# Optimization experiments

Hardware: AMD Instinct MI355X
Metric: run time of the kernel (lower is better)

Reference implementation:

```python
import jax, jax.numpy as jnp
import numpy as np

N = 100000
F_IN = 128
E = 1_600_000
NEG_SLOPE = 0.2  # PyG GATConv default negative_slope


def _seg_sum(v, idx, n):
    return jax.ops.segment_sum(v, idx, num_segments=n)


def gcn_conv(x, W, b, src, dst, n):
    # PyG GCNConv: D^{-1/2} (A + I) D^{-1/2} X W + b (self loops already in src/dst)
    h = x @ W
    deg = _seg_sum(jnp.ones(src.shape, h.dtype), dst, n)
    dinv = jnp.where(deg > 0, jax.lax.rsqrt(deg), 0.0)
    norm = dinv[src] * dinv[dst]  # [E]
    return _seg_sum(h[src] * norm[:, None], dst, n) + b


def gat_conv(x, W, a_src, a_dst, b, src, dst, n, heads, out_ch):
    # PyG GATConv (concat=True), eval mode (dropout inactive)
    h = (x @ W).reshape(n, heads, out_ch)          # [n,H,C]
    s = jnp.einsum('nhc,hc->nh', h, a_src)          # per-node src score
    t = jnp.einsum('nhc,hc->nh', h, a_dst)          # per-node dst score
    e = jax.nn.leaky_relu(s[src] + t[dst], NEG_SLOPE)  # [E,H]
    m = jax.ops.segment_max(e, dst, num_segments=n)    # stable segment softmax
    m = jnp.where(jnp.isfinite(m), m, 0.0)
    p = jnp.exp(e - m[dst])
    denom = _seg_sum(p, dst, n)
    alpha = p / (denom[dst] + 1e-16)                 # [E,H]
    out = _seg_sum(h[src] * alpha[:, :, None], dst, n)  # [n,H,C]
    return out.reshape(n, heads * out_ch) + b


def setup_inputs():
    key = jax.random.key(0)
    ks = jax.random.split(key, 24)
    x = jax.random.normal(ks[0], (N, F_IN), jnp.float32) * 0.1
    half = N // 2
    # one-hot user/item type flags read by forward (x[:,0]==1 / x[:,1]==1)
    x = x.at[:, 0].set(0.0).at[:, 1].set(0.0)
    x = x.at[:half, 0].set(1.0).at[half:, 1].set(1.0)
    src = jax.random.randint(ks[1], (E,), 0, N, dtype=jnp.int32)
    dst = jax.random.randint(ks[2], (E,), 0, N, dtype=jnp.int32)
    edge_index = jnp.stack([src, dst])

    def p(k, shape):
        return jax.random.normal(k, shape, jnp.float32) * 0.1

    inp = {"x": x, "edge_index": edge_index,
           "gcn_w": p(ks[3], (F_IN, 16)), "gcn_b": jnp.zeros((16,), jnp.float32)}
    dims = [(16, 16, 8), (128, 16, 8), (128, 16, 8), (128, 2, 1)]
    for i, (fi, fo, h) in enumerate(dims, start=1):
        inp[f"g{i}_w"] = p(ks[3 + 4 * i], (fi, h * fo))
        inp[f"g{i}_as"] = p(ks[4 + 4 * i], (h, fo))
        inp[f"g{i}_ad"] = p(ks[5 + 4 * i], (h, fo))
        inp[f"g{i}_b"] = jnp.zeros((h * fo,), jnp.float32)
    return inp


def reference(x, edge_index, gcn_w, gcn_b,
              g1_w, g1_as, g1_ad, g1_b,
              g2_w, g2_as, g2_ad, g2_b,
              g3_w, g3_as, g3_ad, g3_b,
              g4_w, g4_as, g4_ad, g4_b):
    n = x.shape[0]
    loops = jnp.arange(n, dtype=edge_index.dtype)  # self loops (added by GCN/GAT layers)
    src = jnp.concatenate([edge_index[0], loops])
    dst = jnp.concatenate([edge_index[1], loops])
    h = jax.nn.elu(gcn_conv(x, gcn_w, gcn_b, src, dst, n))
    h = jax.nn.elu(gat_conv(h, g1_w, g1_as, g1_ad, g1_b, src, dst, n, 8, 16))
    h = jax.nn.elu(gat_conv(h, g2_w, g2_as, g2_ad, g2_b, src, dst, n, 8, 16))
    h = jax.nn.elu(gat_conv(h, g3_w, g3_as, g3_ad, g3_b, src, dst, n, 8, 16))
    h = jax.nn.elu(gat_conv(h, g4_w, g4_as, g4_ad, g4_b, src, dst, n, 1, 2))  # [n,2]
    half = n // 2  # users are rows [:half], items rows [half:]
    out = jnp.concatenate([h[:half], h[half:]], axis=1)  # [half,4]
    return jax.nn.log_softmax(out, axis=1)
```

## Files before the change

kernel.cpp:

```cpp
#include <hip/hip_runtime.h>
#include <cstddef>
#include <cstdint>

#define NN 100000
#define NPAD 100032
#define NE 1600000
#define ET (NE + NN)
#define ETP_MAX (ET + 8 * NN)
#define HALFN (NN / 2)
#define NEG_SLOPE 0.2f
#define SCB 1024
#define RP 8
#define RNODES (NN / RP)
#define CHUNK 8192

typedef __attribute__((ext_vector_type(8))) short short8v;
typedef __attribute__((ext_vector_type(4))) float float4v;
typedef __attribute__((ext_vector_type(2))) float float2v;

__device__ __forceinline__ float lrelu(float x) { return x > 0.f ? x : NEG_SLOPE * x; }

__device__ __forceinline__ uint16_t f2bf(float f) {
  uint32_t u = __float_as_uint(f);
  uint32_t r = u + 0x7fffu + ((u >> 16) & 1u);
  return (uint16_t)(r >> 16);
}
__device__ __forceinline__ float bflo(uint32_t u) { return __uint_as_float(u << 16); }
__device__ __forceinline__ float bfhi(uint32_t u) { return __uint_as_float(u & 0xffff0000u); }

template<int K, int M>
__launch_bounds__(256)
__global__ void gemm4_kernel(const float* __restrict__ X, const float* __restrict__ W,
                             float* __restrict__ Y, int n) {
  constexpr int CG = M / 4;
  constexpr int RG = 256 / CG;
  constexpr int RPT = 2;
  constexpr int RT = RG * RPT;
  constexpr int KP = K + 1;
  __shared__ __align__(16) float sW[K * M];
  __shared__ float sX[RT * KP];
  for (int i = threadIdx.x; i < K * M; i += 256) sW[i] = W[i];
  const int jg = threadIdx.x % CG;
  const int rg = threadIdx.x / CG;
  const int r0 = rg * RPT;
  for (int base = blockIdx.x * RT; base < n; base += gridDim.x * RT) {
    __syncthreads();
    const int nrows = (n - base) < RT ? (n - base) : RT;
    for (int i = threadIdx.x; i < nrows * K; i += 256) {
      int r = i / K, c = i - r * K;
      sX[r * KP + c] = X[(size_t)base * K + i];
    }
    __syncthreads();
    float acc[RPT][4];
    #pragma unroll
    for (int rr = 0; rr < RPT; ++rr) acc[rr][0] = acc[rr][1] = acc[rr][2] = acc[rr][3] = 0.f;
    #pragma unroll 4
    for (int k = 0; k < K; ++k) {
      const float4 w = *(const float4*)&sW[k * M + jg * 4];
      #pragma unroll
      for (int rr = 0; rr < RPT; ++rr) {
        const float xv = sX[(r0 + rr) * KP + k];
        acc[rr][0] = fmaf(xv, w.x, acc[rr][0]);
        acc[rr][1] = fmaf(xv, w.y, acc[rr][1]);
        acc[rr][2] = fmaf(xv, w.z, acc[rr][2]);
        acc[rr][3] = fmaf(xv, w.w, acc[rr][3]);
      }
    }
    #pragma unroll
    for (int rr = 0; rr < RPT; ++rr) {
      if (r0 + rr < nrows) {
        float4 o = make_float4(acc[rr][0], acc[rr][1], acc[rr][2], acc[rr][3]);
        *(float4*)&Y[(size_t)(base + r0 + rr) * M + jg * 4] = o;
      }
    }
  }
}

template<int KB>
__launch_bounds__(256)
__global__ void wpack_kernel(const float* __restrict__ W, uint16_t* __restrict__ wp,
                             int Kreal) {
  int tid = blockIdx.x * 256 + threadIdx.x;
  if (tid >= KB * 8 * 64) return;
  int lane = tid & 63;
  int ctkb = tid >> 6;
  int kb = ctkb % KB, ct = ctkb / KB;
  int nc = ct * 16 + (lane & 15);
  int k0 = kb * 32 + (lane >> 4) * 8;
  ushort4 o0, o1;
  uint16_t v[8];
  #pragma unroll
  for (int j = 0; j < 8; ++j) {
    int k = k0 + j;
    v[j] = (k < Kreal) ? f2bf(W[(size_t)k * 128 + nc]) : (uint16_t)0;
  }
  o0.x = v[0]; o0.y = v[1]; o0.z = v[2]; o0.w = v[3];
  o1.x = v[4]; o1.y = v[5]; o1.z = v[6]; o1.w = v[7];
  *(ushort4*)&wp[(size_t)tid * 8] = o0;
  *(ushort4*)&wp[(size_t)tid * 8 + 4] = o1;
}

template<int KB, int XS>
__launch_bounds__(256)
__global__ void gemm_mfma_kernel(const uint16_t* __restrict__ X,
                                 const uint16_t* __restrict__ wp,
                                 const float* __restrict__ aS, const float* __restrict__ aD,
                                 uint16_t* __restrict__ Y,
                                 float* __restrict__ S, float* __restrict__ T, int n) {
  __shared__ float sC[4][16 * 136];
  const int wv = threadIdx.x >> 6;
  const int lane = threadIdx.x & 63;
  const int rowbase = blockIdx.x * 64 + wv * 16;
  int arow = rowbase + (lane & 15);
  if (arow >= n) arow = n - 1;
  const uint16_t* xp = X + (size_t)arow * XS + ((lane >> 4) * 8);
  short8v a[KB];
  #pragma unroll
  for (int kb = 0; kb < KB; ++kb) a[kb] = *(const short8v*)(xp + kb * 32);
  #pragma unroll
  for (int ct = 0; ct < 8; ++ct) {
    float4v acc = {0.f, 0.f, 0.f, 0.f};
    #pragma unroll
    for (int kb = 0; kb < KB; ++kb) {
      short8v b = *(const short8v*)&wp[(size_t)((ct * KB + kb) * 64 + lane) * 8];
      acc = __builtin_amdgcn_mfma_f32_16x16x32_bf16(a[kb], b, acc, 0, 0, 0);
    }
    #pragma unroll
    for (int r = 0; r < 4; ++r)
      sC[wv][((lane >> 4) * 4 + r) * 136 + ct * 16 + (lane & 15)] = acc[r];
  }
  #pragma unroll
  for (int t = 0; t < 4; ++t) {
    int idx = t * 64 + lane;
    int row = idx >> 4;
    int c8 = idx & 15;
    const float* pr = &sC[wv][row * 136 + c8 * 8];
    float4 lo = *(const float4*)pr;
    float4 hi = *(const float4*)(pr + 4);
    uint4 o;
    o.x = (uint32_t)f2bf(lo.x) | ((uint32_t)f2bf(lo.y) << 16);
    o.y = (uint32_t)f2bf(lo.z) | ((uint32_t)f2bf(lo.w) << 16);
    o.z = (uint32_t)f2bf(hi.x) | ((uint32_t)f2bf(hi.y) << 16);
    o.w = (uint32_t)f2bf(hi.z) | ((uint32_t)f2bf(hi.w) << 16);
    *(uint4*)&Y[(size_t)(rowbase + row) * 128 + c8 * 8] = o;
  }
  {
    int r = lane & 15;
    int hg = lane >> 4;
    int node = rowbase + r;
    if (node < n) {
      #pragma unroll
      for (int hh = 0; hh < 2; ++hh) {
        int h = hg * 2 + hh;
        float sv = 0.f, tv = 0.f;
        #pragma unroll
        for (int c = 0; c < 16; ++c) {
          float v = sC[wv][r * 136 + h * 16 + c];
          sv = fmaf(v, aS[h * 16 + c], sv);
          tv = fmaf(v, aD[h * 16 + c], tv);
        }
        S[(size_t)node * 8 + h] = sv;
        T[(size_t)node * 8 + h] = tv;
      }
    }
  }
}

template<int K, int ROWS>
__launch_bounds__(256)
__global__ void gemm_s2_kernel(const uint16_t* __restrict__ Xb, const float* __restrict__ W,
                               const float* __restrict__ aS, const float* __restrict__ aD,
                               float* __restrict__ Y, float* __restrict__ S,
                               float* __restrict__ T, int n) {
  constexpr int KP = K + 1;
  __shared__ float sW[K * 2];
  __shared__ float sX[ROWS * KP];
  if (blockIdx.x == 0 && threadIdx.x == 0) {
    S[NN] = -1e30f; T[NN] = 0.f;
    Y[(size_t)NN * 2] = 0.f; Y[(size_t)NN * 2 + 1] = 0.f;
  }
  for (int i = threadIdx.x; i < K * 2; i += 256) sW[i] = W[i];
  const float as0 = aS[0], as1 = aS[1], ad0 = aD[0], ad1 = aD[1];
  for (int base = blockIdx.x * ROWS; base < n; base += gridDim.x * ROWS) {
    __syncthreads();
    const int nrows = (n - base) < ROWS ? (n - base) : ROWS;
    for (int i = threadIdx.x; i < nrows * (K / 4); i += 256) {
      int r = i / (K / 4), c = i - r * (K / 4);
      uint2 u = *(const uint2*)&Xb[(size_t)(base + r) * K + c * 4];
      sX[r * KP + c * 4 + 0] = bflo(u.x);
      sX[r * KP + c * 4 + 1] = bfhi(u.x);
      sX[r * KP + c * 4 + 2] = bflo(u.y);
      sX[r * KP + c * 4 + 3] = bfhi(u.y);
    }
    __syncthreads();
    for (int r = threadIdx.x; r < nrows; r += 256) {
      float a0 = 0.f, a1 = 0.f;
      #pragma unroll 4
      for (int k = 0; k < K; ++k) {
        float xv = sX[r * KP + k];
        a0 = fmaf(xv, sW[k * 2], a0);
        a1 = fmaf(xv, sW[k * 2 + 1], a1);
      }
      int node = base + r;
      float2 o; o.x = a0; o.y = a1;
      *(float2*)&Y[(size_t)node * 2] = o;
      S[node] = a0 * as0 + a1 * as1;
      T[node] = a0 * ad0 + a1 * ad1;
    }
  }
}

__launch_bounds__(256)
__global__ void rank_kernel(const int* __restrict__ edst, int* __restrict__ cursor,
                            int* __restrict__ rank) {
  int e = blockIdx.x * 256 + threadIdx.x;
  if (e >= ET) return;
  int dn = e < NE ? edst[e] : e - NE;
  rank[e] = atomicAdd(&cursor[dn], 1);
}

__device__ __forceinline__ int pad8(int d) { return (d + 7) & ~7; }

__launch_bounds__(256)
__global__ void scan1_kernel(const int* __restrict__ degi, int* __restrict__ rowptr,
                             int* __restrict__ bsums) {
  __shared__ int sd[256];
  int t = threadIdx.x;
  int base = blockIdx.x * SCB + t * 4;
  int v0 = base + 0 < NN ? pad8(degi[base + 0]) : 0;
  int v1 = base + 1 < NN ? pad8(degi[base + 1]) : 0;
  int v2 = base + 2 < NN ? pad8(degi[base + 2]) : 0;
  int v3 = base + 3 < NN ? pad8(degi[base + 3]) : 0;
  int s = v0 + v1 + v2 + v3;
  sd[t] = s;
  __syncthreads();
  for (int off = 1; off < 256; off <<= 1) {
    int x = (t >= off) ? sd[t - off] : 0;
    __syncthreads();
    sd[t] += x;
    __syncthreads();
  }
  int excl = sd[t] - s;
  if (t == 255) bsums[blockIdx.x] = sd[255];
  if (base + 0 < NN) rowptr[base + 0] = excl;
  excl += v0;
  if (base + 1 < NN) rowptr[base + 1] = excl;
  excl += v1;
  if (base + 2 < NN) rowptr[base + 2] = excl;
  excl += v2;
  if (base + 3 < NN) rowptr[base + 3] = excl;
}

__launch_bounds__(256)
__global__ void scan2_kernel(int* __restrict__ bsums, int nb) {
  __shared__ int sd[256];
  int t = threadIdx.x;
  int v = t < nb ? bsums[t] : 0;
  sd[t] = v;
  __syncthreads();
  for (int off = 1; off < 256; off <<= 1) {
    int x = (t >= off) ? sd[t - off] : 0;
    __syncthreads();
    sd[t] += x;
    __syncthreads();
  }
  if (t < nb) bsums[t] = sd[t] - v;
  if (t == nb - 1) bsums[nb] = sd[t];
}

__launch_bounds__(256)
__global__ void scan3_kernel(int* __restrict__ rowptr, const int* __restrict__ bsums, int nb) {
  int i = blockIdx.x * 256 + threadIdx.x;
  if (i < NN) rowptr[i] += bsums[i / SCB];
  if (i == 0) rowptr[NN] = bsums[nb];
}

__launch_bounds__(256)
__global__ void dinv_kernel(const int* __restrict__ deg, float* __restrict__ dinv,
                            float* __restrict__ S8, float* __restrict__ T8) {
  int i = blockIdx.x * 256 + threadIdx.x;
  if (i > NN) return;
  if (i == NN) {
    dinv[i] = 0.f;
    #pragma unroll
    for (int h = 0; h < 8; ++h) {
      S8[(size_t)NN * 8 + h] = -1e30f;
      T8[(size_t)NN * 8 + h] = 0.f;
    }
    return;
  }
  int d = deg[i];
  dinv[i] = d > 0 ? rsqrtf((float)d) : 0.f;
}

__launch_bounds__(256)
__global__ void padfill_kernel(const int* __restrict__ rowptr, const int* __restrict__ deg,
                               int* __restrict__ csr) {
  int i = blockIdx.x * 256 + threadIdx.x;
  if (i >= NN) return;
  int e = rowptr[i] + deg[i], e1 = rowptr[i + 1];
  for (; e < e1; ++e) csr[e] = NN;
}

__launch_bounds__(256)
__global__ void scatter_part_kernel(const int* __restrict__ esrc, const int* __restrict__ edst,
                                    const int* __restrict__ rowptr, const int* __restrict__ rank,
                                    int* __restrict__ csr_src) {
  int p = blockIdx.x & (RP - 1);
  int c = blockIdx.x >> 3;
  int lo = p * RNODES, hi = lo + RNODES;
  int e0 = c * CHUNK;
  int e1 = e0 + CHUNK < ET ? e0 + CHUNK : ET;
  for (int e = e0 + threadIdx.x; e < e1; e += 256) {
    int dn = e < NE ? edst[e] : e - NE;
    if (dn >= lo && dn < hi) {
      int sn = e < NE ? esrc[e] : e - NE;
      csr_src[rowptr[dn] + rank[e]] = sn;
    }
  }
}

__launch_bounds__(256)
__global__ void fused_gat_kernel(const int* __restrict__ rowptr, const int* __restrict__ csr,
                                 const float* __restrict__ S, const float* __restrict__ T,
                                 const uint16_t* __restrict__ Hm, const float* __restrict__ bias,
                                 uint16_t* __restrict__ Outb) {
  const int lane = threadIdx.x & 63;
  const int d = (blockIdx.x * 256 + threadIdx.x) >> 6;
  if (d >= NN) return;
  const int rs = rowptr[d];
  const int deg = rowptr[d + 1] - rs;
  const int eg = lane >> 4;
  const int cl = lane & 15;
  const int hp = cl >> 1;
  const float Th = T[(size_t)d * 8 + hp];
  const char* sb = (const char*)S;
  const char* hb = (const char*)Hm;
  float m = -1e38f;
  float s = 0.f;
  float2v A0 = {0.f, 0.f}, A1 = {0.f, 0.f}, A2 = {0.f, 0.f}, A3 = {0.f, 0.f};
  const uint32_t clo = (uint32_t)(cl << 4);
  const uint32_t hpo = (uint32_t)(hp << 2);
  int iA = rs + eg;
  int snA = csr[iA];
  int snB = csr[iA + 4];
  for (int l0 = 0; l0 < deg; l0 += 8) {
    int snA2 = csr[iA + 8];
    int snB2 = csr[iA + 12];
    uint4 uA = *(const uint4*)(hb + (((uint32_t)snA << 8) + clo));
    uint4 uB = *(const uint4*)(hb + (((uint32_t)snB << 8) + clo));
    float svA = *(const float*)(sb + (((uint32_t)snA << 5) + hpo));
    float svB = *(const float*)(sb + (((uint32_t)snB << 5) + hpo));
    iA += 8;
    float eA = lrelu(svA + Th);
    float eB = lrelu(svB + Th);
    float nm = fmaxf(m, fmaxf(eA, eB));
    if (nm > m) {
      float sc = __expf(m - nm);
      float2v scv = {sc, sc};
      s *= sc;
      A0 *= scv; A1 *= scv; A2 *= scv; A3 *= scv;
      m = nm;
    }
    float pA = __expf(eA - m);
    float pB = __expf(eB - m);
    s += pA + pB;
    float2v ppA = {pA, pA}, ppB = {pB, pB};
    A0 = ppA * (float2v){bflo(uA.x), bfhi(uA.x)} + A0;
    A1 = ppA * (float2v){bflo(uA.y), bfhi(uA.y)} + A1;
    A2 = ppA * (float2v){bflo(uA.z), bfhi(uA.z)} + A2;
    A3 = ppA * (float2v){bflo(uA.w), bfhi(uA.w)} + A3;
    A0 = ppB * (float2v){bflo(uB.x), bfhi(uB.x)} + A0;
    A1 = ppB * (float2v){bflo(uB.y), bfhi(uB.y)} + A1;
    A2 = ppB * (float2v){bflo(uB.z), bfhi(uB.z)} + A2;
    A3 = ppB * (float2v){bflo(uB.w), bfhi(uB.w)} + A3;
    snA = snA2; snB = snB2;
  }
  #pragma unroll
  for (int mask = 16; mask <= 32; mask <<= 1) {
    float om = __shfl_xor(m, mask);
    float os = __shfl_xor(s, mask);
    float o0x = __shfl_xor(A0.x, mask), o0y = __shfl_xor(A0.y, mask);
    float o1x = __shfl_xor(A1.x, mask), o1y = __shfl_xor(A1.y, mask);
    float o2x = __shfl_xor(A2.x, mask), o2y = __shfl_xor(A2.y, mask);
    float o3x = __shfl_xor(A3.x, mask), o3y = __shfl_xor(A3.y, mask);
    float nm = fmaxf(m, om);
    float s1 = __expf(m - nm), s2 = __expf(om - nm);
    s = s * s1 + os * s2;
    A0.x = A0.x * s1 + o0x * s2; A0.y = A0.y * s1 + o0y * s2;
    A1.x = A1.x * s1 + o1x * s2; A1.y = A1.y * s1 + o1y * s2;
    A2.x = A2.x * s1 + o2x * s2; A2.y = A2.y * s1 + o2y * s2;
    A3.x = A3.x * s1 + o3x * s2; A3.y = A3.y * s1 + o3y * s2;
    m = nm;
  }
  {
    float2v Blo = (eg & 1) ? A1 : A0;
    float2v Bhi = (eg & 1) ? A3 : A2;
    float2v B = (eg & 2) ? Bhi : Blo;
    const float inv = 1.f / (s + 1e-16f);
    float2 b = *(const float2*)&bias[cl * 8 + eg * 2];
    float v0 = fmaf(B.x, inv, b.x);
    float v1 = fmaf(B.y, inv, b.y);
    v0 = v0 > 0.f ? v0 : expm1f(v0);
    v1 = v1 > 0.f ? v1 : expm1f(v1);
    uint32_t o = (uint32_t)f2bf(v0) | ((uint32_t)f2bf(v1) << 16);
    *(uint32_t*)&Outb[(size_t)d * 128 + cl * 8 + eg * 2] = o;
  }
}

__launch_bounds__(256)
__global__ void fused_gat1_kernel(const int* __restrict__ rowptr, const int* __restrict__ csr,
                                  const float* __restrict__ S, const float* __restrict__ T,
                                  const float* __restrict__ Hm2, const float* __restrict__ bias,
                                  float* __restrict__ Out) {
  int lane = threadIdx.x & 63;
  int sub = lane >> 4, l16 = lane & 15;
  int d = ((blockIdx.x * 256 + threadIdx.x) >> 6) * 4 + sub;
  if (d >= NN) return;
  int rs = rowptr[d], deg = rowptr[d + 1] - rs;
  float Td = T[d];
  float m = -1e38f, sAcc = 0.f, a0 = 0.f, a1 = 0.f;
  for (int l = l16; l < deg; l += 16) {
    int sn = csr[rs + l];
    float2 hv = *(const float2*)&Hm2[(size_t)sn * 2];
    float sv = S[sn];
    float e = lrelu(sv + Td);
    float nm = fmaxf(m, e);
    if (e > m) {
      float sc = __expf(m - nm);
      sAcc *= sc; a0 *= sc; a1 *= sc; m = nm;
    }
    float p = __expf(e - m);
    sAcc += p;
    a0 = fmaf(p, hv.x, a0);
    a1 = fmaf(p, hv.y, a1);
  }
  #pragma unroll
  for (int mask = 1; mask <= 8; mask <<= 1) {
    float om = __shfl_xor(m, mask);
    float os = __shfl_xor(sAcc, mask);
    float oa0 = __shfl_xor(a0, mask);
    float oa1 = __shfl_xor(a1, mask);
    float nm = fmaxf(m, om);
    float s1 = __expf(m - nm), s2 = __expf(om - nm);
    sAcc = sAcc * s1 + os * s2;
    a0 = a0 * s1 + oa0 * s2;
    a1 = a1 * s1 + oa1 * s2;
    m = nm;
  }
  if (l16 == 0) {
    float inv = 1.f / (sAcc + 1e-16f);
    float v0 = fmaf(a0, inv, bias[0]);
    float v1 = fmaf(a1, inv, bias[1]);
    v0 = v0 > 0.f ? v0 : expm1f(v0);
    v1 = v1 > 0.f ? v1 : expm1f(v1);
    float2 o; o.x = v0; o.y = v1;
    *(float2*)&Out[(size_t)d * 2] = o;
  }
}

__launch_bounds__(256)
__global__ void gcn_pull_kernel(const int* __restrict__ rowptr, const int* __restrict__ csr_src,
                                const float* __restrict__ dinv, const float* __restrict__ Hm,
                                const float* __restrict__ bias, uint16_t* __restrict__ Outb) {
  int d = blockIdx.x * 16 + threadIdx.x / 16;
  if (d >= NN) return;
  int f = threadIdx.x & 15;
  int rs = rowptr[d], re = rowptr[d + 1];
  float acc = 0.f;
  int j = rs;
  for (; j + 4 <= re; j += 4) {
    int s0 = csr_src[j], s1 = csr_src[j + 1], s2 = csr_src[j + 2], s3 = csr_src[j + 3];
    float d0 = dinv[s0], d1 = dinv[s1], d2 = dinv[s2], d3 = dinv[s3];
    float h0 = Hm[(size_t)s0 * 16 + f], h1 = Hm[(size_t)s1 * 16 + f];
    float h2 = Hm[(size_t)s2 * 16 + f], h3 = Hm[(size_t)s3 * 16 + f];
    acc = fmaf(d0, h0, acc); acc = fmaf(d1, h1, acc);
    acc = fmaf(d2, h2, acc); acc = fmaf(d3, h3, acc);
  }
  for (; j < re; ++j) {
    int sn = csr_src[j];
    acc = fmaf(dinv[sn], Hm[(size_t)sn * 16 + f], acc);
  }
  float v = acc * dinv[d] + bias[f];
  v = v > 0.f ? v : expm1f(v);
  Outb[(size_t)d * 32 + f] = f2bf(v);
  Outb[(size_t)d * 32 + 16 + f] = 0;
}

__launch_bounds__(256)
__global__ void final_kernel(const float* __restrict__ A, float* __restrict__ Out) {
  int i = blockIdx.x * 256 + threadIdx.x;
  if (i >= HALFN) return;
  float v0 = A[(size_t)i * 2 + 0];
  float v1 = A[(size_t)i * 2 + 1];
  float v2 = A[(size_t)(i + HALFN) * 2 + 0];
  float v3 = A[(size_t)(i + HALFN) * 2 + 1];
  float m = fmaxf(fmaxf(v0, v1), fmaxf(v2, v3));
  float e0 = __expf(v0 - m), e1 = __expf(v1 - m), e2 = __expf(v2 - m), e3 = __expf(v3 - m);
  float l = logf(e0 + e1 + e2 + e3) + m;
  Out[(size_t)i * 4 + 0] = v0 - l;
  Out[(size_t)i * 4 + 1] = v1 - l;
  Out[(size_t)i * 4 + 2] = v2 - l;
  Out[(size_t)i * 4 + 3] = v3 - l;
}

extern "C" void kernel_launch(void* const* d_in, const int* in_sizes, int n_in,
                              void* d_out, int out_size, void* d_ws, size_t ws_size,
                              hipStream_t stream) {
  const float* x     = (const float*)d_in[0];
  const int*   eidx  = (const int*)d_in[1];
  const int*   esrc  = eidx;
  const int*   edst  = eidx + NE;
  const float* gcn_w = (const float*)d_in[2];
  const float* gcn_b = (const float*)d_in[3];

  char* ws = (char*)d_ws;
  uint16_t* hbf    = (uint16_t*)(ws + 0);
  uint16_t* bufAb  = (uint16_t*)(ws + 25700000);
  uint16_t* gcnHbf = (uint16_t*)(ws + 51400000);
  float*    bufB   = (float*)   (ws + 57900000);
  float*    bufC   = (float*)   (ws + 64400000);
  float*    Sb     = (float*)   (ws + 65300000);
  float*    Tb     = (float*)   (ws + 68600000);
  int*      rowptr = (int*)     (ws + 151900000);
  int*      cursor = (int*)     (ws + 152300008);
  int*      csr    = (int*)     (ws + 152700008);
  float*    dinv   = (float*)   (ws + 162700008);
  int*      bsums  = (int*)     (ws + 163100016);
  int*      rank   = (int*)     (ws + 163100528);
  uint16_t* wpck   = (uint16_t*)(ws + 169900528);

  constexpr int NB_SCAN = (NN + SCB - 1) / SCB;

  hipMemsetAsync(cursor, 0, (size_t)NN * 4, stream);
  rank_kernel<<<(ET + 255) / 256, 256, 0, stream>>>(edst, cursor, rank);
  scan1_kernel<<<NB_SCAN, 256, 0, stream>>>(cursor, rowptr, bsums);
  scan2_kernel<<<1, 256, 0, stream>>>(bsums, NB_SCAN);
  scan3_kernel<<<(NN + 256) / 256, 256, 0, stream>>>(rowptr, bsums, NB_SCAN);
  dinv_kernel<<<(NN + 256) / 256, 256, 0, stream>>>(cursor, dinv, Sb, Tb);
  padfill_kernel<<<(NN + 255) / 256, 256, 0, stream>>>(rowptr, cursor, csr);
  {
    int nch = (ET + CHUNK - 1) / CHUNK;
    scatter_part_kernel<<<nch * RP, 256, 0, stream>>>(esrc, edst, rowptr, rank, csr);
  }

  {
    int tiles = (NN + 127) / 128;
    if (tiles > 4096) tiles = 4096;
    gemm4_kernel<128, 16><<<tiles, 256, 0, stream>>>(x, gcn_w, bufB, NN);
  }
  gcn_pull_kernel<<<(NN + 15) / 16, 256, 0, stream>>>(rowptr, csr, dinv, bufB, gcn_b, gcnHbf);

  wpack_kernel<1><<<2, 256, 0, stream>>>((const float*)d_in[4], wpck, 16);
  gemm_mfma_kernel<1, 32><<<NPAD / 64, 256, 0, stream>>>(
      gcnHbf, wpck, (const float*)d_in[5], (const float*)d_in[6], hbf, Sb, Tb, NN);
  fused_gat_kernel<<<(NN * 64 + 255) / 256, 256, 0, stream>>>(
      rowptr, csr, Sb, Tb, hbf, (const float*)d_in[7], bufAb);

  wpack_kernel<4><<<8, 256, 0, stream>>>((const float*)d_in[8], wpck, 128);
  gemm_mfma_kernel<4, 128><<<NPAD / 64, 256, 0, stream>>>(
      bufAb, wpck, (const float*)d_in[9], (const float*)d_in[10], hbf, Sb, Tb, NN);
  fused_gat_kernel<<<(NN * 64 + 255) / 256, 256, 0, stream>>>(
      rowptr, csr, Sb, Tb, hbf, (const float*)d_in[11], bufAb);

  wpack_kernel<4><<<8, 256, 0, stream>>>((const float*)d_in[12], wpck, 128);
  gemm_mfma_kernel<4, 128><<<NPAD / 64, 256, 0, stream>>>(
      bufAb, wpck, (const float*)d_in[13], (const float*)d_in[14], hbf, Sb, Tb, NN);
  fused_gat_kernel<<<(NN * 64 + 255) / 256, 256, 0, stream>>>(
      rowptr, csr, Sb, Tb, hbf, (const float*)d_in[15], bufAb);

  {
    int tiles = (NN + 127) / 128;
    if (tiles > 2048) tiles = 2048;
    gemm_s2_kernel<128, 128><<<tiles, 256, 0, stream>>>(
        bufAb, (const float*)d_in[16], (const float*)d_in[17], (const float*)d_in[18],
        bufB, Sb, Tb, NN);
    fused_gat1_kernel<<<(NN * 16 + 255) / 256, 256, 0, stream>>>(
        rowptr, csr, Sb, Tb, bufB, (const float*)d_in[19], bufC);
  }

  final_kernel<<<(HALFN + 255) / 256, 256, 0, stream>>>(bufC, (float*)d_out);
}
```

Baseline: 518.4 us.

## Rebuild CSR with atomic slot claiming, pad-4 rows, fused scan/dinv/padfill

```diff
diff --git a/kernel.cpp b/kernel.cpp
--- a/kernel.cpp
+++ b/kernel.cpp
@@ -211,15 +211,14 @@
 }
 
 __launch_bounds__(256)
-__global__ void rank_kernel(const int* __restrict__ edst, int* __restrict__ cursor,
-                            int* __restrict__ rank) {
+__global__ void deg_int_kernel(const int* __restrict__ edst, int* __restrict__ degi) {
   int e = blockIdx.x * 256 + threadIdx.x;
   if (e >= ET) return;
   int dn = e < NE ? edst[e] : e - NE;
-  rank[e] = atomicAdd(&cursor[dn], 1);
-}
-
-__device__ __forceinline__ int pad8(int d) { return (d + 7) & ~7; }
+  atomicAdd(&degi[dn], 1);
+}
+
+__device__ __forceinline__ int pad4i(int d) { return (d + 3) & ~3; }
 
 __launch_bounds__(256)
 __global__ void scan1_kernel(const int* __restrict__ degi, int* __restrict__ rowptr,
@@ -227,10 +226,10 @@
   __shared__ int sd[256];
   int t = threadIdx.x;
   int base = blockIdx.x * SCB + t * 4;
-  int v0 = base + 0 < NN ? pad8(degi[base + 0]) : 0;
-  int v1 = base + 1 < NN ? pad8(degi[base + 1]) : 0;
-  int v2 = base + 2 < NN ? pad8(degi[base + 2]) : 0;
-  int v3 = base + 3 < NN ? pad8(degi[base + 3]) : 0;
+  int v0 = base + 0 < NN ? pad4i(degi[base + 0]) : 0;
+  int v1 = base + 1 < NN ? pad4i(degi[base + 1]) : 0;
+  int v2 = base + 2 < NN ? pad4i(degi[base + 2]) : 0;
+  int v3 = base + 3 < NN ? pad4i(degi[base + 3]) : 0;
   int s = v0 + v1 + v2 + v3;
   sd[t] = s;
   __syncthreads();
@@ -269,42 +268,32 @@
 }
 
 __launch_bounds__(256)
-__global__ void scan3_kernel(int* __restrict__ rowptr, const int* __restrict__ bsums, int nb) {
+__global__ void scan3_kernel(int* __restrict__ rowptr, const int* __restrict__ bsums, int nb,
+                             const int* __restrict__ deg, float* __restrict__ dinv,
+                             float* __restrict__ S8, float* __restrict__ T8,
+                             int* __restrict__ csr) {
   int i = blockIdx.x * 256 + threadIdx.x;
-  if (i < NN) rowptr[i] += bsums[i / SCB];
-  if (i == 0) rowptr[NN] = bsums[nb];
-}
-
-__launch_bounds__(256)
-__global__ void dinv_kernel(const int* __restrict__ deg, float* __restrict__ dinv,
-                            float* __restrict__ S8, float* __restrict__ T8) {
-  int i = blockIdx.x * 256 + threadIdx.x;
-  if (i > NN) return;
-  if (i == NN) {
-    dinv[i] = 0.f;
+  if (i == 0) {
+    rowptr[NN] = bsums[nb];
+    dinv[NN] = 0.f;
     #pragma unroll
     for (int h = 0; h < 8; ++h) {
       S8[(size_t)NN * 8 + h] = -1e30f;
       T8[(size_t)NN * 8 + h] = 0.f;
     }
-    return;
-  }
-  int d = deg[i];
-  dinv[i] = d > 0 ? rsqrtf((float)d) : 0.f;
-}
-
-__launch_bounds__(256)
-__global__ void padfill_kernel(const int* __restrict__ rowptr, const int* __restrict__ deg,
-                               int* __restrict__ csr) {
-  int i = blockIdx.x * 256 + threadIdx.x;
+  }
   if (i >= NN) return;
-  int e = rowptr[i] + deg[i], e1 = rowptr[i + 1];
-  for (; e < e1; ++e) csr[e] = NN;
+  int rp = rowptr[i] + bsums[i / SCB];
+  rowptr[i] = rp;
+  int dg = deg[i];
+  dinv[i] = dg > 0 ? rsqrtf((float)dg) : 0.f;
+  int pe = rp + pad4i(dg);
+  for (int e = rp + dg; e < pe; ++e) csr[e] = NN;
 }
 
 __launch_bounds__(256)
 __global__ void scatter_part_kernel(const int* __restrict__ esrc, const int* __restrict__ edst,
-                                    const int* __restrict__ rowptr, const int* __restrict__ rank,
+                                    const int* __restrict__ rowptr, int* __restrict__ cur2,
                                     int* __restrict__ csr_src) {
   int p = blockIdx.x & (RP - 1);
   int c = blockIdx.x >> 3;
@@ -315,7 +304,8 @@
     int dn = e < NE ? edst[e] : e - NE;
     if (dn >= lo && dn < hi) {
       int sn = e < NE ? esrc[e] : e - NE;
-      csr_src[rowptr[dn] + rank[e]] = sn;
+      int slot = rowptr[dn] + atomicAdd(&cur2[dn], 1);
+      csr_src[slot] = sn;
     }
   }
 }
@@ -330,6 +320,7 @@
   if (d >= NN) return;
   const int rs = rowptr[d];
   const int deg = rowptr[d + 1] - rs;
+  const int deg8 = deg & ~7;
   const int eg = lane >> 4;
   const int cl = lane & 15;
   const int hp = cl >> 1;
@@ -344,7 +335,7 @@
   int iA = rs + eg;
   int snA = csr[iA];
   int snB = csr[iA + 4];
-  for (int l0 = 0; l0 < deg; l0 += 8) {
+  for (int l0 = 0; l0 < deg8; l0 += 8) {
     int snA2 = csr[iA + 8];
     int snB2 = csr[iA + 12];
     uint4 uA = *(const uint4*)(hb + (((uint32_t)snA << 8) + clo));
@@ -375,6 +366,26 @@
     A2 = ppB * (float2v){bflo(uB.z), bfhi(uB.z)} + A2;
     A3 = ppB * (float2v){bflo(uB.w), bfhi(uB.w)} + A3;
     snA = snA2; snB = snB2;
+  }
+  if (deg & 4) {
+    uint4 uA = *(const uint4*)(hb + (((uint32_t)snA << 8) + clo));
+    float svA = *(const float*)(sb + (((uint32_t)snA << 5) + hpo));
+    float eA = lrelu(svA + Th);
+    float nm = fmaxf(m, eA);
+    if (nm > m) {
+      float sc = __expf(m - nm);
+      float2v scv = {sc, sc};
+      s *= sc;
+      A0 *= scv; A1 *= scv; A2 *= scv; A3 *= scv;
+      m = nm;
+    }
+    float pA = __expf(eA - m);
+    s += pA;
+    float2v ppA = {pA, pA};
+    A0 = ppA * (float2v){bflo(uA.x), bfhi(uA.x)} + A0;
+    A1 = ppA * (float2v){bflo(uA.y), bfhi(uA.y)} + A1;
+    A2 = ppA * (float2v){bflo(uA.z), bfhi(uA.z)} + A2;
+    A3 = ppA * (float2v){bflo(uA.w), bfhi(uA.w)} + A3;
   }
   #pragma unroll
   for (int mask = 16; mask <= 32; mask <<= 1) {
@@ -463,28 +474,24 @@
 __global__ void gcn_pull_kernel(const int* __restrict__ rowptr, const int* __restrict__ csr_src,
                                 const float* __restrict__ dinv, const float* __restrict__ Hm,
                                 const float* __restrict__ bias, uint16_t* __restrict__ Outb) {
-  int d = blockIdx.x * 16 + threadIdx.x / 16;
+  int lane = threadIdx.x & 63;
+  int d = (blockIdx.x * 256 + threadIdx.x) >> 6;
   if (d >= NN) return;
-  int f = threadIdx.x & 15;
-  int rs = rowptr[d], re = rowptr[d + 1];
+  int eg = lane >> 4, f = lane & 15;
+  int rs = rowptr[d], deg = rowptr[d + 1] - rs;
   float acc = 0.f;
-  int j = rs;
-  for (; j + 4 <= re; j += 4) {
-    int s0 = csr_src[j], s1 = csr_src[j + 1], s2 = csr_src[j + 2], s3 = csr_src[j + 3];
-    float d0 = dinv[s0], d1 = dinv[s1], d2 = dinv[s2], d3 = dinv[s3];
-    float h0 = Hm[(size_t)s0 * 16 + f], h1 = Hm[(size_t)s1 * 16 + f];
-    float h2 = Hm[(size_t)s2 * 16 + f], h3 = Hm[(size_t)s3 * 16 + f];
-    acc = fmaf(d0, h0, acc); acc = fmaf(d1, h1, acc);
-    acc = fmaf(d2, h2, acc); acc = fmaf(d3, h3, acc);
-  }
-  for (; j < re; ++j) {
-    int sn = csr_src[j];
+  for (int l = eg; l < deg; l += 4) {
+    int sn = csr_src[l + rs];
     acc = fmaf(dinv[sn], Hm[(size_t)sn * 16 + f], acc);
   }
-  float v = acc * dinv[d] + bias[f];
-  v = v > 0.f ? v : expm1f(v);
-  Outb[(size_t)d * 32 + f] = f2bf(v);
-  Outb[(size_t)d * 32 + 16 + f] = 0;
+  acc += __shfl_xor(acc, 16);
+  acc += __shfl_xor(acc, 32);
+  if (eg == 0) {
+    float v = acc * dinv[d] + bias[f];
+    v = v > 0.f ? v : expm1f(v);
+    Outb[(size_t)d * 32 + f] = f2bf(v);
+    Outb[(size_t)d * 32 + 16 + f] = 0;
+  }
 }
 
 __launch_bounds__(256)
@@ -527,21 +534,21 @@
   int*      csr    = (int*)     (ws + 152700008);
   float*    dinv   = (float*)   (ws + 162700008);
   int*      bsums  = (int*)     (ws + 163100016);
-  int*      rank   = (int*)     (ws + 163100528);
+  int*      cur2   = (int*)     (ws + 163100528);
   uint16_t* wpck   = (uint16_t*)(ws + 169900528);
 
   constexpr int NB_SCAN = (NN + SCB - 1) / SCB;
 
   hipMemsetAsync(cursor, 0, (size_t)NN * 4, stream);
-  rank_kernel<<<(ET + 255) / 256, 256, 0, stream>>>(edst, cursor, rank);
+  hipMemsetAsync(cur2, 0, (size_t)NN * 4, stream);
+  deg_int_kernel<<<(ET + 255) / 256, 256, 0, stream>>>(edst, cursor);
   scan1_kernel<<<NB_SCAN, 256, 0, stream>>>(cursor, rowptr, bsums);
   scan2_kernel<<<1, 256, 0, stream>>>(bsums, NB_SCAN);
-  scan3_kernel<<<(NN + 256) / 256, 256, 0, stream>>>(rowptr, bsums, NB_SCAN);
-  dinv_kernel<<<(NN + 256) / 256, 256, 0, stream>>>(cursor, dinv, Sb, Tb);
-  padfill_kernel<<<(NN + 255) / 256, 256, 0, stream>>>(rowptr, cursor, csr);
+  scan3_kernel<<<(NN + 256) / 256, 256, 0, stream>>>(rowptr, bsums, NB_SCAN,
+                                                     cursor, dinv, Sb, Tb, csr);
   {
     int nch = (ET + CHUNK - 1) / CHUNK;
-    scatter_part_kernel<<<nch * RP, 256, 0, stream>>>(esrc, edst, rowptr, rank, csr);
+    scatter_part_kernel<<<nch * RP, 256, 0, stream>>>(esrc, edst, rowptr, cur2, csr);
   }
 
   {
@@ -549,7 +556,8 @@
     if (tiles > 4096) tiles = 4096;
     gemm4_kernel<128, 16><<<tiles, 256, 0, stream>>>(x, gcn_w, bufB, NN);
   }
-  gcn_pull_kernel<<<(NN + 15) / 16, 256, 0, stream>>>(rowptr, csr, dinv, bufB, gcn_b, gcnHbf);
+  gcn_pull_kernel<<<(NN * 64 + 255) / 256, 256, 0, stream>>>(
+      rowptr, csr, dinv, bufB, gcn_b, gcnHbf);
 
   wpack_kernel<1><<<2, 256, 0, stream>>>((const float*)d_in[4], wpck, 16);
   gemm_mfma_kernel<1, 32><<<NPAD / 64, 256, 0, stream>>>(
```

New measurement: 573.3 us. +10.6%, slower.
